# Optimization experiments

Hardware: AMD Instinct MI355X
Metric: run time of the kernel (lower is better)

Reference implementation:

```python
import jax, jax.numpy as jnp
import numpy as np

KH = KW = 3
SH = SW = 1
DH = DW = 1

def _same_padding(ih, iw):
    eff_kh = (KH - 1) * DH + 1
    eff_kw = (KW - 1) * DW + 1
    out_h = (ih + SH - 1) // SH
    out_w = (iw + SW - 1) // SW
    pad_h = max((out_h - 1) * SH + eff_kh - ih, 0)
    pad_w = max((out_w - 1) * SW + eff_kw - iw, 0)
    pad_top = pad_h // 2
    pad_bottom = pad_h - pad_top
    pad_left = pad_w // 2
    pad_right = pad_w - pad_left
    return (pad_top, pad_bottom), (pad_left, pad_right)


def setup_inputs() -> dict:
    key = jax.random.key(0)
    k1, k2, k3 = jax.random.split(key, 3)
    N, C, H, Wd = 32, 192, 56, 56
    Cout = 384
    x = jax.random.normal(k1, (N, C, H, Wd), dtype=jnp.float32)
    # linear weight (Cout, C*KH*KW) with unfold ordering (c, kh, kw) -> OIHW kernel
    W = jax.random.normal(k2, (Cout, C, KH, KW), dtype=jnp.float32) * (1.0 / np.sqrt(C * KH * KW))
    b = jax.random.normal(k3, (Cout,), dtype=jnp.float32) * 0.01
    return {"x": x, "W": W, "b": b}


def reference(x, W, b):
    # ConvLayer: F.pad('same') -> nn.Unfold -> Linear -> reshape, which is
    # mathematically a 2D conv with OIHW kernel W (unfold orders features as c,kh,kw).
    _, _, H, Wd = x.shape
    pad_hw = _same_padding(H, Wd)
    out = jax.lax.conv_general_dilated(
        x, W,
        window_strides=(SH, SW),
        padding=pad_hw,
        rhs_dilation=(DH, DW),
        dimension_numbers=("NCHW", "OIHW", "NCHW"),
    )
    return out + b[None, :, None, None]
```

## Files before the change

kernel.cpp:

```cpp
#include <hip/hip_runtime.h>
#include <cstdint>
#include <cstddef>

#define N_IMG 32
#define C_IN 192
#define HW 56
#define SPAT (HW*HW)
#define C_OUT 384
#define HP 58
#define KPOS 9

#define BM 128
#define BN 128
#define BK 64
#define NTILE_S 25
#define NTILE_CO 3
#define GRID_MAIN (N_IMG*NTILE_CO*NTILE_S)

typedef __attribute__((ext_vector_type(8))) short short8;
typedef __attribute__((ext_vector_type(4))) float f32x4;

__device__ __forceinline__ unsigned short f2bf(float f) {
  union { float f; unsigned u; } v; v.f = f;
  unsigned u = v.u;
  unsigned r = (u + 0x7FFFu + ((u >> 16) & 1u)) >> 16;
  return (unsigned short)r;
}

__device__ __forceinline__ void async_load16(const void* gsrc, void* ldst) {
  __builtin_amdgcn_global_load_lds(
      (const __attribute__((address_space(1))) unsigned int*)gsrc,
      (__attribute__((address_space(3))) unsigned int*)ldst,
      16, 0, 0);
}

__global__ void pack_w(const float* __restrict__ W, unsigned short* __restrict__ Wp) {
  int idx = blockIdx.x*256 + threadIdx.x;
  if (idx >= C_OUT*KPOS*C_IN) return;
  int c   = idx % C_IN;
  int pos = (idx / C_IN) % KPOS;
  int co  = idx / (C_IN*KPOS);
  float v = W[((size_t)co*C_IN + c)*KPOS + pos];
  Wp[idx] = f2bf(v);
}

__global__ void zero_border(unsigned short* __restrict__ Xp) {
  int idx = blockIdx.x*256 + threadIdx.x;
  if (idx >= N_IMG*228*C_IN) return;
  int c    = idx % C_IN;
  int cell = (idx / C_IN) % 228;
  int n    = idx / (C_IN*228);
  int hh, ww;
  if (cell < 116) { hh = (cell < 58) ? 0 : 57; ww = cell % 58; }
  else { int b2 = cell - 116; ww = (b2 < 56) ? 0 : 57; hh = 1 + (b2 % 56); }
  Xp[(((size_t)n*HP + hh)*HP + ww)*C_IN + c] = 0;
}

__global__ void pack_x(const float* __restrict__ x, unsigned short* __restrict__ Xp) {
  __shared__ float tile[64*57];
  int b  = blockIdx.x;
  int cb = b % 3;
  int h  = (b/3) % HW;
  int n  = b / (3*HW);
  int tid = threadIdx.x;
  const float* src = x + (size_t)n*C_IN*SPAT + (size_t)cb*64*SPAT + h*HW;
  #pragma unroll
  for (int i = 0; i < 14; ++i) {
    int idx = i*256 + tid;
    int c = idx / HW, w = idx % HW;
    tile[c*57 + w] = src[(size_t)c*SPAT + w];
  }
  __syncthreads();
  unsigned short* dst = Xp + (((size_t)n*HP + h + 1)*HP + 1)*C_IN + cb*64;
  #pragma unroll
  for (int i = 0; i < 14; ++i) {
    int idx = i*256 + tid;
    int w = idx / 64, c = idx % 64;
    dst[(size_t)w*C_IN + c] = f2bf(tile[c*57 + w]);
  }
}

__global__ __launch_bounds__(256) void conv_gemm(
    const unsigned short* __restrict__ Wp,
    const unsigned short* __restrict__ Xp,
    const float* __restrict__ bias,
    float* __restrict__ out)
{
  __shared__ __attribute__((aligned(16))) unsigned short As[BM*BK];
  __shared__ __attribute__((aligned(16))) unsigned short Bs[BN*BK];

  int bid = blockIdx.x;
  int logical = (bid & 7) * (GRID_MAIN/8) + (bid >> 3);
  int cotile = logical % NTILE_CO;
  int rest   = logical / NTILE_CO;
  int stile  = rest % NTILE_S;
  int n      = rest / NTILE_S;

  const int tid  = threadIdx.x;
  const int lane = tid & 63;
  const int wv   = tid >> 6;
  const int l7   = lane & 7;
  const int l3   = lane >> 3;
  const int lanep = lane & 15;
  const int laneq = lane >> 4;
  const int gsl  = ((l7 ^ l3) << 3);

  size_t aBase[4];
  size_t bBase[4];
  #pragma unroll
  for (int i = 0; i < 4; ++i) {
    int r  = (wv*4 + i)*8 + l3;
    int co = cotile*BM + r;
    aBase[i] = ((size_t)co*KPOS)*C_IN + gsl;
    int sg = stile*BN + r;
    if (sg > SPAT-1) sg = SPAT-1;
    int hh = sg / HW, ww = sg % HW;
    bBase[i] = (((size_t)n*HP + hh)*HP + ww)*C_IN + gsl;
  }

  const int aoff0 = (((wv>>1)*64 + lanep) << 6) + ((laneq ^ l7) << 3);
  const int boff0 = (((wv&1)*64 + lanep) << 6) + ((laneq ^ l7) << 3);

  f32x4 acc[4][4];
  #pragma unroll
  for (int mf = 0; mf < 4; ++mf)
    #pragma unroll
    for (int nf = 0; nf < 4; ++nf)
      acc[mf][nf] = (f32x4){0.f, 0.f, 0.f, 0.f};

  for (int pos = 0; pos < KPOS; ++pos) {
    const int kh = pos / 3, kw = pos % 3;
    const size_t posOff = ((size_t)kh*HP + kw)*C_IN;
    for (int c0 = 0; c0 < C_IN; c0 += BK) {
      __syncthreads();
      #pragma unroll
      for (int i = 0; i < 4; ++i) {
        async_load16(Wp + aBase[i] + pos*C_IN + c0, &As[(wv*4 + i)*512]);
        async_load16(Xp + bBase[i] + posOff   + c0, &Bs[(wv*4 + i)*512]);
      }
      __syncthreads();
      #pragma unroll
      for (int kk = 0; kk < 2; ++kk) {
        const int kx = kk << 5;
        short8 av[4], bv[4];
        #pragma unroll
        for (int mf = 0; mf < 4; ++mf)
          av[mf] = *(const short8*)&As[(aoff0 + mf*1024) ^ kx];
        #pragma unroll
        for (int nf = 0; nf < 4; ++nf)
          bv[nf] = *(const short8*)&Bs[(boff0 + nf*1024) ^ kx];
        #pragma unroll
        for (int mf = 0; mf < 4; ++mf)
          #pragma unroll
          for (int nf = 0; nf < 4; ++nf)
            acc[mf][nf] = __builtin_amdgcn_mfma_f32_16x16x32_bf16(
                av[mf], bv[nf], acc[mf][nf], 0, 0, 0);
      }
    }
  }

  const int coB = cotile*BM + (wv>>1)*64;
  const int sB  = stile*BN + (wv&1)*64;
  #pragma unroll
  for (int mf = 0; mf < 4; ++mf) {
    #pragma unroll
    for (int i = 0; i < 4; ++i) {
      int co = coB + mf*16 + laneq*4 + i;
      float bi = bias[co];
      float* orow = out + ((size_t)n*C_OUT + co)*SPAT;
      #pragma unroll
      for (int nf = 0; nf < 4; ++nf) {
        int s = sB + nf*16 + lanep;
        if (s < SPAT) orow[s] = acc[mf][nf][i] + bi;
      }
    }
  }
}

__global__ void conv_naive(const float* __restrict__ x, const float* __restrict__ W,
                           const float* __restrict__ bias, float* __restrict__ out) {
  size_t idx = (size_t)blockIdx.x*256 + threadIdx.x;
  if (idx >= (size_t)N_IMG*C_OUT*SPAT) return;
  int s  = idx % SPAT;
  int co = (int)((idx / SPAT) % C_OUT);
  int n  = (int)(idx / ((size_t)SPAT*C_OUT));
  int h = s / HW, w = s % HW;
  float acc = bias[co];
  for (int c = 0; c < C_IN; ++c) {
    for (int kh = 0; kh < 3; ++kh) {
      int hh = h + kh - 1;
      if (hh < 0 || hh >= HW) continue;
      for (int kw = 0; kw < 3; ++kw) {
        int ww = w + kw - 1;
        if (ww < 0 || ww >= HW) continue;
        acc += x[(((size_t)n*C_IN + c)*HW + hh)*HW + ww]
             * W[(((size_t)co*C_IN + c)*3 + kh)*3 + kw];
      }
    }
  }
  out[idx] = acc;
}

extern "C" void kernel_launch(void* const* d_in, const int* in_sizes, int n_in,
                              void* d_out, int out_size, void* d_ws, size_t ws_size,
                              hipStream_t stream) {
  const float* x = (const float*)d_in[0];
  const float* W = (const float*)d_in[1];
  const float* b = (const float*)d_in[2];
  float* out = (float*)d_out;

  const size_t WP_ELEMS = (size_t)C_OUT*KPOS*C_IN;
  const size_t XP_ELEMS = (size_t)N_IMG*HP*HP*C_IN;
  const size_t NEED = (WP_ELEMS + XP_ELEMS)*2;

  if (ws_size >= NEED) {
    unsigned short* Wp = (unsigned short*)d_ws;
    unsigned short* Xp = Wp + WP_ELEMS;
    zero_border<<<(N_IMG*228*C_IN + 255)/256, 256, 0, stream>>>(Xp);
    pack_w<<<(int)((WP_ELEMS + 255)/256), 256, 0, stream>>>(W, Wp);
    pack_x<<<N_IMG*HW*3, 256, 0, stream>>>(x, Xp);
    conv_gemm<<<GRID_MAIN, 256, 0, stream>>>(Wp, Xp, b, out);
  } else {
    size_t total = (size_t)N_IMG*C_OUT*SPAT;
    conv_naive<<<(int)((total + 255)/256), 256, 0, stream>>>(x, W, b, out);
  }
}
```

Baseline: 204.9 us.

## Pipeline conv GEMM with 4-slot LDS ring, 512-thread blocks, flattened batch tiles

Rewrites the implicit-GEMM conv kernel to use 512-thread workgroups computing 128x256 tiles. The spatial dimension is flattened across the batch so tiles no longer waste the padded tail. The K loop is split into 54 steps of 32 channels, fed by a 4-slot LDS ring with three stages in flight and explicit vmcnt waits, so global-to-LDS loads overlap MFMA work instead of sitting behind two syncthreads per step. It also raises MFMA priority during the compute phase. In exchange, LDS use grows to about 96KB per block, and the hand-placed waits and barriers must match the number of loads in flight.

```diff
diff --git a/kernel.cpp b/kernel.cpp
--- a/kernel.cpp
+++ b/kernel.cpp
@@ -5,17 +5,18 @@
 #define N_IMG 32
 #define C_IN 192
 #define HW 56
-#define SPAT (HW*HW)
+#define SPAT 3136
 #define C_OUT 384
 #define HP 58
 #define KPOS 9
+#define KTOT 1728
+#define NSUB 54
 
 #define BM 128
-#define BN 128
-#define BK 64
-#define NTILE_S 25
-#define NTILE_CO 3
-#define GRID_MAIN (N_IMG*NTILE_CO*NTILE_S)
+#define BN 256
+#define NT_CO 3
+#define NT_S  392
+#define GRID_MAIN (NT_CO*NT_S)
 
 typedef __attribute__((ext_vector_type(8))) short short8;
 typedef __attribute__((ext_vector_type(4))) float f32x4;
@@ -80,46 +81,53 @@
   }
 }
 
-__global__ __launch_bounds__(256) void conv_gemm(
+__global__ __launch_bounds__(512, 2) void conv_gemm(
     const unsigned short* __restrict__ Wp,
     const unsigned short* __restrict__ Xp,
     const float* __restrict__ bias,
     float* __restrict__ out)
 {
-  __shared__ __attribute__((aligned(16))) unsigned short As[BM*BK];
-  __shared__ __attribute__((aligned(16))) unsigned short Bs[BN*BK];
+  __shared__ __attribute__((aligned(16))) unsigned short lds[4][12288];
 
   int bid = blockIdx.x;
-  int logical = (bid & 7) * (GRID_MAIN/8) + (bid >> 3);
-  int cotile = logical % NTILE_CO;
-  int rest   = logical / NTILE_CO;
-  int stile  = rest % NTILE_S;
-  int n      = rest / NTILE_S;
-
-  const int tid  = threadIdx.x;
-  const int lane = tid & 63;
-  const int wv   = tid >> 6;
-  const int l7   = lane & 7;
-  const int l3   = lane >> 3;
+  int wg = (bid & 7) * (GRID_MAIN/8) + (bid >> 3);
+  int cotile = wg % NT_CO;
+  int stile  = wg / NT_CO;
+
+  const int tid   = threadIdx.x;
+  const int lane  = tid & 63;
+  const int wv    = tid >> 6;
+  const int wm    = wv >> 2;
+  const int wn    = wv & 3;
   const int lanep = lane & 15;
   const int laneq = lane >> 4;
-  const int gsl  = ((l7 ^ l3) << 3);
-
-  size_t aBase[4];
-  size_t bBase[4];
-  #pragma unroll
-  for (int i = 0; i < 4; ++i) {
-    int r  = (wv*4 + i)*8 + l3;
-    int co = cotile*BM + r;
-    aBase[i] = ((size_t)co*KPOS)*C_IN + gsl;
-    int sg = stile*BN + r;
-    if (sg > SPAT-1) sg = SPAT-1;
-    int hh = sg / HW, ww = sg % HW;
-    bBase[i] = (((size_t)n*HP + hh)*HP + ww)*C_IN + gsl;
-  }
-
-  const int aoff0 = (((wv>>1)*64 + lanep) << 6) + ((laneq ^ l7) << 3);
-  const int boff0 = (((wv&1)*64 + lanep) << 6) + ((laneq ^ l7) << 3);
+  const int l2    = lane >> 2;
+  const int l4    = lane & 3;
+  const int chunkSw = l4 ^ (l2 & 3);
+
+  const int aRow = cotile*BM + wv*16 + l2;
+  const unsigned short* aSrc = Wp + (size_t)aRow*KTOT + chunkSw*8;
+
+  const unsigned short* bSrc0;
+  const unsigned short* bSrc1;
+  {
+    int r0 = (wv*2 + 0)*16 + l2;
+    int f0 = stile*BN + r0;
+    int n0 = f0 / SPAT, sp0 = f0 % SPAT;
+    bSrc0 = Xp + (((size_t)n0*HP + sp0/HW)*HP + sp0%HW)*C_IN + chunkSw*8;
+    int r1 = (wv*2 + 1)*16 + l2;
+    int f1 = stile*BN + r1;
+    int n1 = f1 / SPAT, sp1 = f1 % SPAT;
+    bSrc1 = Xp + (((size_t)n1*HP + sp1/HW)*HP + sp1%HW)*C_IN + chunkSw*8;
+  }
+
+  unsigned short* aDst  = &lds[0][wv*512];
+  unsigned short* bDst0 = &lds[0][4096 + (wv*2 + 0)*512];
+  unsigned short* bDst1 = &lds[0][4096 + (wv*2 + 1)*512];
+
+  const int swz8   = (laneq ^ (lanep & 3)) << 3;
+  const int aRdBase = (wm*64 + lanep)*32 + swz8;
+  const int bRdBase = 4096 + (wn*64 + lanep)*32 + swz8;
 
   f32x4 acc[4][4];
   #pragma unroll
@@ -128,50 +136,71 @@
     for (int nf = 0; nf < 4; ++nf)
       acc[mf][nf] = (f32x4){0.f, 0.f, 0.f, 0.f};
 
-  for (int pos = 0; pos < KPOS; ++pos) {
-    const int kh = pos / 3, kw = pos % 3;
-    const size_t posOff = ((size_t)kh*HP + kw)*C_IN;
-    for (int c0 = 0; c0 < C_IN; c0 += BK) {
-      __syncthreads();
+  auto bOffOf = [](int t) {
+    int kh = t / 18;
+    int r  = t - kh*18;
+    int kw = r / 6;
+    int c6 = r - kw*6;
+    return (kh*HP + kw)*C_IN + c6*32;
+  };
+
+  auto stage = [&](int t) {
+    int slot = t & 3;
+    async_load16(aSrc + t*32, aDst + slot*12288);
+    int bo = bOffOf(t);
+    async_load16(bSrc0 + bo, bDst0 + slot*12288);
+    async_load16(bSrc1 + bo, bDst1 + slot*12288);
+  };
+
+#define PHASE(sv, VMC, DO_STAGE)                                            \
+  {                                                                         \
+    asm volatile("s_waitcnt vmcnt(" #VMC ")" ::: "memory");                 \
+    __builtin_amdgcn_s_barrier();                                           \
+    __builtin_amdgcn_sched_barrier(0);                                      \
+    const int slot_ = (sv) & 3;                                             \
+    const unsigned short* la_ = &lds[slot_][0];                             \
+    short8 av_[4], bv_[4];                                                  \
+    _Pragma("unroll")                                                       \
+    for (int mf = 0; mf < 4; ++mf)                                          \
+      av_[mf] = *(const short8*)&la_[aRdBase + mf*512];                     \
+    _Pragma("unroll")                                                       \
+    for (int nf = 0; nf < 4; ++nf)                                          \
+      bv_[nf] = *(const short8*)&la_[bRdBase + nf*512];                     \
+    if (DO_STAGE) stage((sv) + 3);                                          \
+    __builtin_amdgcn_s_setprio(1);                                          \
+    _Pragma("unroll")                                                       \
+    for (int mf = 0; mf < 4; ++mf)                                          \
+      _Pragma("unroll")                                                     \
+      for (int nf = 0; nf < 4; ++nf)                                        \
+        acc[mf][nf] = __builtin_amdgcn_mfma_f32_16x16x32_bf16(              \
+            av_[mf], bv_[nf], acc[mf][nf], 0, 0, 0);                        \
+    __builtin_amdgcn_s_setprio(0);                                          \
+    __builtin_amdgcn_sched_barrier(0);                                      \
+  }
+
+  stage(0); stage(1); stage(2);
+
+  for (int s = 0; s < 51; ++s)
+    PHASE(s, 6, true);
+  PHASE(51, 6, false);
+  PHASE(52, 3, false);
+  PHASE(53, 0, false);
+#undef PHASE
+
+  const int coB = cotile*BM + wm*64;
+  const int fB  = stile*BN + wn*64;
+  #pragma unroll
+  for (int nf = 0; nf < 4; ++nf) {
+    int f  = fB + nf*16 + lanep;
+    int n  = f / SPAT;
+    int sp = f % SPAT;
+    float* obase = out + (size_t)n*C_OUT*SPAT + sp;
+    #pragma unroll
+    for (int mf = 0; mf < 4; ++mf) {
       #pragma unroll
       for (int i = 0; i < 4; ++i) {
-        async_load16(Wp + aBase[i] + pos*C_IN + c0, &As[(wv*4 + i)*512]);
-        async_load16(Xp + bBase[i] + posOff   + c0, &Bs[(wv*4 + i)*512]);
-      }
-      __syncthreads();
-      #pragma unroll
-      for (int kk = 0; kk < 2; ++kk) {
-        const int kx = kk << 5;
-        short8 av[4], bv[4];
-        #pragma unroll
-        for (int mf = 0; mf < 4; ++mf)
-          av[mf] = *(const short8*)&As[(aoff0 + mf*1024) ^ kx];
-        #pragma unroll
-        for (int nf = 0; nf < 4; ++nf)
-          bv[nf] = *(const short8*)&Bs[(boff0 + nf*1024) ^ kx];
-        #pragma unroll
-        for (int mf = 0; mf < 4; ++mf)
-          #pragma unroll
-          for (int nf = 0; nf < 4; ++nf)
-            acc[mf][nf] = __builtin_amdgcn_mfma_f32_16x16x32_bf16(
-                av[mf], bv[nf], acc[mf][nf], 0, 0, 0);
-      }
-    }
-  }
-
-  const int coB = cotile*BM + (wv>>1)*64;
-  const int sB  = stile*BN + (wv&1)*64;
-  #pragma unroll
-  for (int mf = 0; mf < 4; ++mf) {
-    #pragma unroll
-    for (int i = 0; i < 4; ++i) {
-      int co = coB + mf*16 + laneq*4 + i;
-      float bi = bias[co];
-      float* orow = out + ((size_t)n*C_OUT + co)*SPAT;
-      #pragma unroll
-      for (int nf = 0; nf < 4; ++nf) {
-        int s = sB + nf*16 + lanep;
-        if (s < SPAT) orow[s] = acc[mf][nf][i] + bi;
+        int co = coB + mf*16 + laneq*4 + i;
+        obase[(size_t)co*SPAT] = acc[mf][nf][i] + bias[co];
       }
     }
   }
@@ -186,7 +215,7 @@
   int n  = (int)(idx / ((size_t)SPAT*C_OUT));
   int h = s / HW, w = s % HW;
   float acc = bias[co];
-  for (int c = 0; c < C_IN; ++c) {
+  for (int c = 0; c < C_IN; ++c)
     for (int kh = 0; kh < 3; ++kh) {
       int hh = h + kh - 1;
       if (hh < 0 || hh >= HW) continue;
@@ -197,7 +226,6 @@
              * W[(((size_t)co*C_IN + c)*3 + kh)*3 + kw];
       }
     }
-  }
   out[idx] = acc;
 }
 
@@ -219,7 +247,7 @@
     zero_border<<<(N_IMG*228*C_IN + 255)/256, 256, 0, stream>>>(Xp);
     pack_w<<<(int)((WP_ELEMS + 255)/256), 256, 0, stream>>>(W, Wp);
     pack_x<<<N_IMG*HW*3, 256, 0, stream>>>(x, Xp);
-    conv_gemm<<<GRID_MAIN, 256, 0, stream>>>(Wp, Xp, b, out);
+    conv_gemm<<<GRID_MAIN, 512, 0, stream>>>(Wp, Xp, b, out);
   } else {
     size_t total = (size_t)N_IMG*C_OUT*SPAT;
     conv_naive<<<(int)((total + 255)/256), 256, 0, stream>>>(x, W, b, out);
```

New measurement: 186.4 us. 9.0% less time.
